# Kernel optimization log

Measured on AMD Instinct MI355X. Metric: run time of the kernel, lower is better.

The kernel has to match this reference:

```python
import jax, jax.numpy as jnp
import numpy as np

B, T_AUDIO, D_IN = 64, 500, 768
H = 1024
NUM_CHARS = 1024  # must equal H: one-hot char embeddings feed the LSTM input
SEQ_LEN = 128


def setup_inputs() -> dict:
    key = jax.random.key(0)
    ks = jax.random.split(key, 16)
    s = 1.0 / np.sqrt(H)
    u = lambda k, shape: jax.random.uniform(k, shape, jnp.float32, -s, s)
    return {
        "audio_features": jax.random.normal(ks[0], (B, T_AUDIO, D_IN), jnp.float32),
        "text_indices": jax.random.randint(ks[1], (B, SEQ_LEN), 0, NUM_CHARS),
        "W_proj": u(ks[2], (H, D_IN)), "b_proj": u(ks[3], (H,)),
        "W_ih0": u(ks[4], (4 * H, H)), "W_hh0": u(ks[5], (4 * H, H)),
        "b_ih0": u(ks[6], (4 * H,)), "b_hh0": u(ks[7], (4 * H,)),
        "W_ih1": u(ks[8], (4 * H, H)), "W_hh1": u(ks[9], (4 * H, H)),
        "b_ih1": u(ks[10], (4 * H,)), "b_hh1": u(ks[11], (4 * H,)),
        "W_out": u(ks[12], (NUM_CHARS, H)), "b_out": u(ks[13], (NUM_CHARS,)),
    }


def _lstm_cell(x, h, c, W_ih, W_hh, b_ih, b_hh):
    # PyTorch gate order: i, f, g, o
    g = x @ W_ih.T + h @ W_hh.T + b_ih + b_hh
    i, f, gg, o = jnp.split(g, 4, axis=-1)
    c = jax.nn.sigmoid(f) * c + jax.nn.sigmoid(i) * jnp.tanh(gg)
    h = jax.nn.sigmoid(o) * jnp.tanh(c)
    return h, c


def reference(audio_features, text_indices, W_proj, b_proj,
              W_ih0, W_hh0, b_ih0, b_hh0,
              W_ih1, W_hh1, b_ih1, b_hh1,
              W_out, b_out):
    # audio encoding: project then mean-pool over time -> [B, H]
    audio_enc = jnp.mean(audio_features @ W_proj.T + b_proj, axis=1)
    seq_len = text_indices.shape[1]
    # teacher-forcing inputs: step 0 = audio encoding, steps 1..L-1 = one-hot of
    # text_indices[:, 1:seq_len-1] (NUM_CHARS == H)
    one_hots = jax.nn.one_hot(text_indices[:, 1:seq_len - 1], NUM_CHARS,
                              dtype=audio_enc.dtype)  # [B, L-1, H]
    xs = jnp.concatenate([audio_enc[:, None, :], one_hots], axis=1)  # [B, L, H]
    xs = jnp.swapaxes(xs, 0, 1)  # [L, B, H]
    z = jnp.zeros((audio_enc.shape[0], H), audio_enc.dtype)

    def step(carry, x):
        h0, c0, h1, c1 = carry
        h0, c0 = _lstm_cell(x, h0, c0, W_ih0, W_hh0, b_ih0, b_hh0)
        h1, c1 = _lstm_cell(h0, h1, c1, W_ih1, W_hh1, b_ih1, b_hh1)
        return (h0, c0, h1, c1), h1

    _, hs = jax.lax.scan(step, (z, z, z, z), xs)  # hs: [L, B, H]
    outs = jnp.swapaxes(hs, 0, 1)  # [B, L, H]
    logits = outs @ W_out.T + b_out  # [B, L, NUM_CHARS]
    return logits
```

## Files before the change

kernel.cpp:

```cpp
#include <hip/hip_runtime.h>
#include <hip/hip_bf16.h>

#define HH     1024
#define BB     64
#define DIN    768
#define TAUD   500
#define LSTEPS 127
#define G4     4096
#define NB     256
#define BHH    (BB*HH)

typedef __attribute__((ext_vector_type(8))) short bf16x8;
typedef __attribute__((ext_vector_type(4))) float f32x4;
typedef unsigned short u16;
typedef unsigned long long u64;

__device__ __forceinline__ u16 f2b(float x){
  __hip_bfloat16 h = __float2bfloat16(x);
  return __builtin_bit_cast(u16, h);
}
__device__ __forceinline__ float b2f(u16 u){
  unsigned int x = ((unsigned int)u) << 16;
  return __builtin_bit_cast(float, x);
}
__device__ __forceinline__ float sig_(float x){ return 1.0f/(1.0f+__expf(-x)); }
__device__ __forceinline__ float tanh_(float x){
  float ax = fabsf(x);
  float e  = __expf(-2.0f*ax);
  float t  = (1.0f-e)/(1.0f+e);
  return x < 0.0f ? -t : t;
}

constexpr size_t O_PACK  = 0;
constexpr size_t O_WG    = O_PACK + (size_t)NB*3*16384*2;
constexpr size_t O_WOHI  = O_WG   + (size_t)NB*16384*2;
constexpr size_t O_WOLO  = O_WOHI + (size_t)HH*HH*2;
constexpr size_t O_B0P   = O_WOLO + (size_t)HH*HH*2;
constexpr size_t O_B1P   = O_B0P  + G4*4;
constexpr size_t O_G0    = O_B1P  + G4*4;
constexpr size_t O_MEAN  = O_G0   + (size_t)BB*HH*4*4;
constexpr size_t O_X0    = O_MEAN + (size_t)BB*DIN*4;
constexpr size_t O_H0R   = O_X0   + (size_t)BHH*2;
constexpr size_t O_HS    = O_H0R  + (size_t)LSTEPS*BHH*2;
constexpr size_t O_BAR   = O_HS   + (size_t)LSTEPS*BHH*2;

__global__ void init_kernel(int* bar){
  if (threadIdx.x < 512) bar[threadIdx.x] = 0;
}

__global__ void pool_kernel(const float* __restrict__ audio, float* __restrict__ mean){
  int b = blockIdx.x/3, dc = blockIdx.x%3;
  int d = dc*256 + threadIdx.x;
  const float* p = audio + (size_t)b*TAUD*DIN + d;
  float s = 0.f;
  #pragma unroll 5
  for (int t=0;t<TAUD;++t) s += p[(size_t)t*DIN];
  mean[b*DIN + d] = s*(1.0f/TAUD);
}

__global__ void project_kernel(const float* __restrict__ mean, const float* __restrict__ Wp,
                               const float* __restrict__ bp, u16* __restrict__ x0){
  __shared__ float wrow[DIN];
  __shared__ float part[256];
  int h = blockIdx.x;
  for (int i=threadIdx.x;i<DIN;i+=256) wrow[i] = Wp[(size_t)h*DIN + i];
  __syncthreads();
  int b = threadIdx.x>>2, q = threadIdx.x&3;
  const float* mr = mean + b*DIN + q*192;
  const float* wr = wrow + q*192;
  float s = 0.f;
  #pragma unroll 8
  for (int i=0;i<192;++i) s += mr[i]*wr[i];
  part[threadIdx.x] = s;
  __syncthreads();
  if (q==0){
    float v = part[threadIdx.x]+part[threadIdx.x+1]+part[threadIdx.x+2]+part[threadIdx.x+3] + bp[h];
    x0[b*HH + h] = f2b(v);
  }
}

__global__ void g0_kernel(const float* __restrict__ Wih0, const u16* __restrict__ x0bf,
                          float* __restrict__ G0p){
  __shared__ float wr[4][HH];
  __shared__ float part[256][4];
  int u = blockIdx.x;
  for (int i=threadIdx.x; i<4*HH; i+=256){
    int g = i>>10, k = i&1023;
    wr[g][k] = b2f(f2b(Wih0[(size_t)(u + g*HH)*HH + k]));
  }
  __syncthreads();
  int b = threadIdx.x>>2, q = threadIdx.x&3;
  const u16* xr = x0bf + b*HH + q*256;
  float s0=0,s1=0,s2=0,s3=0;
  for (int k=0;k<256;++k){
    float xv = b2f(xr[k]);
    s0 += xv*wr[0][q*256+k]; s1 += xv*wr[1][q*256+k];
    s2 += xv*wr[2][q*256+k]; s3 += xv*wr[3][q*256+k];
  }
  part[threadIdx.x][0]=s0; part[threadIdx.x][1]=s1;
  part[threadIdx.x][2]=s2; part[threadIdx.x][3]=s3;
  __syncthreads();
  if (threadIdx.x < 64){
    int bb = threadIdx.x;
    #pragma unroll
    for (int g=0;g<4;++g){
      float v = part[bb*4][g]+part[bb*4+1][g]+part[bb*4+2][g]+part[bb*4+3][g];
      G0p[((size_t)bb*HH + u)*4 + g] = v;
    }
  }
}

__global__ void pack_w_kernel(const float* __restrict__ Whh0, const float* __restrict__ Wih1,
                              const float* __restrict__ Whh1, u16* __restrict__ P){
  int bid = blockIdx.x, m = blockIdx.y;
  const float* src = (m==0)? Whh0 : (m==1)? Wih1 : Whh1;
  u16* dst = P + ((size_t)bid*3 + m)*16384;
  for (int e = threadIdx.x; e < 16384; e += 256){
    int r = e&31, col = (e>>5)&15, ktg = e>>9;
    int ng = bid*4 + (col&3) + (col>>2)*HH;
    dst[e] = f2b(src[(size_t)ng*HH + ktg*32 + r]);
  }
}

__global__ void pack_wg_kernel(const float* __restrict__ Wih0, u16* __restrict__ WG){
  int bid = blockIdx.x;
  for (int i = threadIdx.x; i < 16384; i += 256){
    int ch = i>>4, u = (i>>2)&3, g = i&3;
    WG[(size_t)bid*16384 + i] = f2b(Wih0[(size_t)(bid*4 + u + g*HH)*HH + ch]);
  }
}

__global__ void pack_bias_kernel(const float* bih0, const float* bhh0,
                                 const float* bih1, const float* bhh1,
                                 float* B0p, float* B1p){
  int i = blockIdx.x*256 + threadIdx.x;
  if (i < G4){
    int n = (i>>2) + (i&3)*HH;
    B0p[i] = bih0[n]+bhh0[n];
    B1p[i] = bih1[n]+bhh1[n];
  }
}

__global__ void wout_kernel(const float* __restrict__ src, u16* __restrict__ hi,
                            u16* __restrict__ lo, int n){
  int i = blockIdx.x*256+threadIdx.x, st = gridDim.x*256;
  for (;i<n;i+=st){
    float v = src[i];
    u16 h = f2b(v);
    hi[i] = h;
    lo[i] = f2b(v - b2f(h));
  }
}

__device__ __forceinline__ void sysst32(unsigned* p, unsigned v){
  __hip_atomic_store(p, v, __ATOMIC_RELAXED, __HIP_MEMORY_SCOPE_SYSTEM);
}

__device__ __forceinline__ void gridbar(int* bar, int t){
  __syncthreads();
  if (threadIdx.x==0){
    int leaf = blockIdx.x>>4;
    int a = __hip_atomic_fetch_add(&bar[leaf*32], 1, __ATOMIC_RELAXED, __HIP_MEMORY_SCOPE_SYSTEM);
    int r = a - t*16;
    if (r == 15)
      __hip_atomic_fetch_add(&bar[511], 1, __ATOMIC_RELAXED, __HIP_MEMORY_SCOPE_SYSTEM);
    if (r == 0 || r == 15){
      while (__hip_atomic_load(&bar[511], __ATOMIC_RELAXED, __HIP_MEMORY_SCOPE_SYSTEM) < (t+1)*16)
        __builtin_amdgcn_s_sleep(4);
      if (r == 0)
        __hip_atomic_store(&bar[leaf*32+16], t+1, __ATOMIC_RELAXED, __HIP_MEMORY_SCOPE_SYSTEM);
    } else {
      while (__hip_atomic_load(&bar[leaf*32+16], __ATOMIC_RELAXED, __HIP_MEMORY_SCOPE_SYSTEM) < t+1)
        __builtin_amdgcn_s_sleep(4);
    }
    asm volatile("" ::: "memory");
  }
  __syncthreads();
}

__device__ __forceinline__ f32x4 gemmK(const u16* __restrict__ A, const u16* B, f32x4 acc){
  #pragma unroll
  for (int h=0; h<2; ++h){
    bf16x8 af[16];
    #pragma unroll
    for (int i=0;i<16;++i) af[i] = *(const bf16x8*)(A + (h*16+i)*32);
    #pragma unroll
    for (int i=0;i<16;++i)
      acc = __builtin_amdgcn_mfma_f32_16x16x32_bf16(af[i], *(const bf16x8*)(B + (h*16+i)*512), acc, 0,0,0);
  }
  return acc;
}
__device__ __forceinline__ f32x4 gemm2K(const u16* __restrict__ A1, const u16* __restrict__ A2,
                                        const u16* B1, const u16* B2){
  f32x4 a1 = {0,0,0,0}, a2 = {0,0,0,0};
  #pragma unroll
  for (int h=0; h<2; ++h){
    bf16x8 af[16], ag[16];
    #pragma unroll
    for (int i=0;i<16;++i) af[i] = *(const bf16x8*)(A1 + (h*16+i)*32);
    #pragma unroll
    for (int i=0;i<16;++i) ag[i] = *(const bf16x8*)(A2 + (h*16+i)*32);
    #pragma unroll
    for (int i=0;i<16;++i){
      a1 = __builtin_amdgcn_mfma_f32_16x16x32_bf16(af[i], *(const bf16x8*)(B1 + (h*16+i)*512), a1, 0,0,0);
      a2 = __builtin_amdgcn_mfma_f32_16x16x32_bf16(ag[i], *(const bf16x8*)(B2 + (h*16+i)*512), a2, 0,0,0);
    }
  }
  return a1 + a2;
}

__device__ __forceinline__ void xpose(const f32x4 acc, float* gv, int lane){
  const int base = lane & 48, up = (lane>>2)&3, r = lane&3;
  #pragma unroll
  for (int g=0; g<4; ++g){
    int src = base | (g*4 + up);
    float v0 = __shfl(acc[0], src);
    float v1 = __shfl(acc[1], src);
    float v2 = __shfl(acc[2], src);
    float v3 = __shfl(acc[3], src);
    gv[g] = (r==0)? v0 : (r==1)? v1 : (r==2)? v2 : v3;
  }
}

__global__ void __launch_bounds__(256, 1) lstm_kernel(
    const u16* __restrict__ P, const u16* __restrict__ WG,
    const float* __restrict__ B0p, const float* __restrict__ B1p,
    const float* __restrict__ G0p, const int* __restrict__ tix,
    u16* __restrict__ h0r, u16* __restrict__ hs, int* __restrict__ bar)
{
  extern __shared__ char smem[];
  u16* Plds = (u16*)smem;
  u16* WGl  = (u16*)(smem + 98304);
  u16* tixl = (u16*)(smem + 98304 + 32768);

  const int tid  = threadIdx.x;
  const int lane = tid&63, mg = tid>>6, quad = lane>>4, colc = lane&15;
  const int bid  = blockIdx.x;

  {
    const bf16x8* gs = (const bf16x8*)(P + (size_t)bid*49152);
    bf16x8* gd = (bf16x8*)Plds;
    #pragma unroll
    for (int i=0;i<24;++i) gd[tid + i*256] = gs[tid + i*256];
    const bf16x8* ws = (const bf16x8*)(WG + (size_t)bid*16384);
    bf16x8* wd = (bf16x8*)WGl;
    #pragma unroll
    for (int i=0;i<8;++i) wd[tid + i*256] = ws[tid + i*256];
    for (int i=tid; i<BB*128; i+=256) tixl[i] = (u16)tix[(i&63)*128 + (i>>6)];
  }

  const int aoff = (mg*16 + colc)*HH + quad*8;
  const int boff = colc*32 + quad*8;
  const u16* B_hh0 = Plds + boff;
  const u16* B_ih1 = Plds + 16384 + boff;
  const u16* B_hh1 = Plds + 2*16384 + boff;

  const int bT = mg*16 + quad*4 + (lane&3);
  const int up = (lane>>2)&3;
  const int ug = bid*4 + up;
  const float4 vb0 = *(const float4*)(B0p + ug*4);
  const float4 vb1 = *(const float4*)(B1p + ug*4);
  float cc0 = 0.f, cc1 = 0.f;
  __syncthreads();

  {
    float4 g0 = *(const float4*)(G0p + ((size_t)bT*HH + ug)*4);
    float gi = g0.x+vb0.x, gg = g0.z+vb0.z, go = g0.w+vb0.w;
    cc0 = sig_(gi)*tanh_(gg);
    unsigned hv = f2b(sig_(go)*tanh_(cc0));
    unsigned ov = __shfl_xor(hv, 4);
    if ((lane&4)==0)
      sysst32((unsigned*)h0r + (bT*HH + ug)/2, hv | (ov<<16));
  }

  #pragma unroll 1
  for (int t=0;t<LSTEPS;++t){
    gridbar(bar, t);
    const u16* A1 = h0r + (size_t)t*BHH + aoff;
    {
      f32x4 acc;
      if (t==0){
        f32x4 z = {0,0,0,0};
        acc = gemmK(A1, B_ih1, z);
      } else {
        acc = gemm2K(A1, hs + (size_t)(t-1)*BHH + aoff, B_ih1, B_hh1);
      }
      float gv[4];
      xpose(acc, gv, lane);
      gv[0]+=vb1.x; gv[1]+=vb1.y; gv[2]+=vb1.z; gv[3]+=vb1.w;
      cc1 = sig_(gv[1])*cc1 + sig_(gv[0])*tanh_(gv[2]);
      unsigned hv = f2b(sig_(gv[3])*tanh_(cc1));
      unsigned ov = __shfl_xor(hv, 4);
      if ((lane&4)==0)
        sysst32((unsigned*)hs + (((size_t)t*BB + bT)*HH + ug)/2, hv | (ov<<16));
    }
    if (t < LSTEPS-1){
      f32x4 z = {0,0,0,0};
      f32x4 acc = gemmK(A1, B_hh0, z);
      float gv[4];
      xpose(acc, gv, lane);
      int ch = tixl[(t+1)*64 + bT];
      ushort4 wv = *(const ushort4*)(WGl + ch*16 + up*4);
      gv[0]+=vb0.x+b2f(wv.x); gv[1]+=vb0.y+b2f(wv.y);
      gv[2]+=vb0.z+b2f(wv.z); gv[3]+=vb0.w+b2f(wv.w);
      cc0 = sig_(gv[1])*cc0 + sig_(gv[0])*tanh_(gv[2]);
      unsigned hv = f2b(sig_(gv[3])*tanh_(cc0));
      unsigned ov = __shfl_xor(hv, 4);
      if ((lane&4)==0)
        sysst32((unsigned*)(h0r + (size_t)(t+1)*BHH) + (bT*HH + ug)/2, hv | (ov<<16));
    }
  }
}

__global__ void __launch_bounds__(512) logits_kernel(
    const u16* __restrict__ hs, const u16* __restrict__ Whi, const u16* __restrict__ Wlo,
    const float* __restrict__ bout, float* __restrict__ out)
{
  extern __shared__ u16 bsh[];
  const int tid = threadIdx.x;
  const int w = tid>>6, lane = tid&63, quad = lane>>4, col = lane&15;
  const int mt = blockIdx.x*8 + w;
  const bool active = (mt < (LSTEPS*BB)/16);
  bf16x8 afr[32];
  if (active){
    const u16* ap = hs + (size_t)(mt*16+col)*HH + quad*8;
    #pragma unroll
    for (int kt=0;kt<32;++kt) afr[kt] = *(const bf16x8*)(ap + kt*32);
  }
  const int nt0 = blockIdx.y*16;
  for (int nt=nt0; nt<nt0+16; ++nt){
    __syncthreads();
    #pragma unroll
    for (int i=0;i<8;++i){
      int cid = i*512 + tid;
      int mat = cid>>11;
      int r = (cid>>7)&15, ck = cid&127;
      const u16* src = (mat? Wlo : Whi) + (size_t)(nt*16+r)*HH + ck*8;
      *(bf16x8*)(bsh + mat*16512 + r*1032 + ck*8) = *(const bf16x8*)src;
    }
    __syncthreads();
    if (active){
      f32x4 acc = {0.f,0.f,0.f,0.f};
      const u16* bh = bsh + col*1032 + quad*8;
      const u16* bl = bsh + 16512 + col*1032 + quad*8;
      #pragma unroll 8
      for (int kt=0;kt<32;++kt){
        bf16x8 b1 = *(const bf16x8*)(bh + kt*32);
        acc = __builtin_amdgcn_mfma_f32_16x16x32_bf16(afr[kt], b1, acc, 0,0,0);
        bf16x8 b2 = *(const bf16x8*)(bl + kt*32);
        acc = __builtin_amdgcn_mfma_f32_16x16x32_bf16(afr[kt], b2, acc, 0,0,0);
      }
      float bb = bout[nt*16 + col];
      #pragma unroll
      for (int r=0;r<4;++r){
        int m = mt*16 + quad*4 + r;
        int tt = m>>6, b_ = m&63;
        out[((size_t)b_*LSTEPS + tt)*HH + nt*16 + col] = acc[r] + bb;
      }
    }
  }
}

extern "C" void kernel_launch(void* const* d_in, const int* in_sizes, int n_in,
                              void* d_out, int out_size, void* d_ws, size_t ws_size,
                              hipStream_t stream) {
  const float* audio = (const float*)d_in[0];
  const int*   tix   = (const int*)  d_in[1];
  const float* Wproj = (const float*)d_in[2];
  const float* bproj = (const float*)d_in[3];
  const float* Wih0  = (const float*)d_in[4];
  const float* Whh0  = (const float*)d_in[5];
  const float* bih0  = (const float*)d_in[6];
  const float* bhh0  = (const float*)d_in[7];
  const float* Wih1  = (const float*)d_in[8];
  const float* Whh1  = (const float*)d_in[9];
  const float* bih1  = (const float*)d_in[10];
  const float* bhh1  = (const float*)d_in[11];
  const float* Wout  = (const float*)d_in[12];
  const float* bout  = (const float*)d_in[13];
  float* out = (float*)d_out;

  char* ws = (char*)d_ws;
  u16*   wP    = (u16*)  (ws + O_PACK);
  u16*   wWG   = (u16*)  (ws + O_WG);
  u16*   wWoHi = (u16*)  (ws + O_WOHI);
  u16*   wWoLo = (u16*)  (ws + O_WOLO);
  float* wB0p  = (float*)(ws + O_B0P);
  float* wB1p  = (float*)(ws + O_B1P);
  float* wG0   = (float*)(ws + O_G0);
  float* wMean = (float*)(ws + O_MEAN);
  u16*   wX0   = (u16*)  (ws + O_X0);
  u16*   wH0R  = (u16*)  (ws + O_H0R);
  u16*   wHS   = (u16*)  (ws + O_HS);
  int*   wBar  = (int*)  (ws + O_BAR);

  init_kernel<<<1, 512, 0, stream>>>(wBar);
  pool_kernel<<<BB*3, 256, 0, stream>>>(audio, wMean);
  project_kernel<<<HH, 256, 0, stream>>>(wMean, Wproj, bproj, wX0);
  g0_kernel<<<HH, 256, 0, stream>>>(Wih0, wX0, wG0);
  pack_w_kernel<<<dim3(NB,3), 256, 0, stream>>>(Whh0, Wih1, Whh1, wP);
  pack_wg_kernel<<<NB, 256, 0, stream>>>(Wih0, wWG);
  pack_bias_kernel<<<16, 256, 0, stream>>>(bih0, bhh0, bih1, bhh1, wB0p, wB1p);
  wout_kernel<<<512, 256, 0, stream>>>(Wout, wWoHi, wWoLo, HH*HH);
  lstm_kernel<<<NB, 256, 98304 + 32768 + 16384, stream>>>(
      wP, wWG, wB0p, wB1p, wG0, tix, wH0R, wHS, wBar);
  logits_kernel<<<dim3(64,4), 512, 66048, stream>>>(wHS, wWoHi, wWoLo, bout, out);
}
```

Before: 2.438 ms.

## Replace hierarchical grid barrier with per-step flag arrays and split-layer waits

Replaces the atomic-counter tree barrier in the persistent LSTM kernel with per-block, per-step u16 ready flags for each layer. A wavefront polls all 256 flags at once with 64-bit loads. The step is reordered so layer 0's next hidden state is computed and published first. Layer 1 then waits only on the previous step's layer-1 flags, so the two layers can overlap instead of sharing one full barrier per step. This removes serialized atomic contention but adds more flag memory and two poll points per step.

```diff
diff --git a/kernel.cpp b/kernel.cpp
--- a/kernel.cpp
+++ b/kernel.cpp
@@ -42,10 +42,13 @@
 constexpr size_t O_X0    = O_MEAN + (size_t)BB*DIN*4;
 constexpr size_t O_H0R   = O_X0   + (size_t)BHH*2;
 constexpr size_t O_HS    = O_H0R  + (size_t)LSTEPS*BHH*2;
-constexpr size_t O_BAR   = O_HS   + (size_t)LSTEPS*BHH*2;
-
-__global__ void init_kernel(int* bar){
-  if (threadIdx.x < 512) bar[threadIdx.x] = 0;
+constexpr size_t O_FLA   = O_HS   + (size_t)LSTEPS*BHH*2;
+constexpr size_t O_FLB   = O_FLA  + 65536;
+
+__global__ void init_kernel(int* fl){
+  int i = blockIdx.x*256 + threadIdx.x;
+  int st = gridDim.x*256;
+  for (int k=i; k<32768; k+=st) fl[k] = 0;
 }
 
 __global__ void pool_kernel(const float* __restrict__ audio, float* __restrict__ mean){
@@ -155,27 +158,17 @@
 __device__ __forceinline__ void sysst32(unsigned* p, unsigned v){
   __hip_atomic_store(p, v, __ATOMIC_RELAXED, __HIP_MEMORY_SCOPE_SYSTEM);
 }
-
-__device__ __forceinline__ void gridbar(int* bar, int t){
-  __syncthreads();
-  if (threadIdx.x==0){
-    int leaf = blockIdx.x>>4;
-    int a = __hip_atomic_fetch_add(&bar[leaf*32], 1, __ATOMIC_RELAXED, __HIP_MEMORY_SCOPE_SYSTEM);
-    int r = a - t*16;
-    if (r == 15)
-      __hip_atomic_fetch_add(&bar[511], 1, __ATOMIC_RELAXED, __HIP_MEMORY_SCOPE_SYSTEM);
-    if (r == 0 || r == 15){
-      while (__hip_atomic_load(&bar[511], __ATOMIC_RELAXED, __HIP_MEMORY_SCOPE_SYSTEM) < (t+1)*16)
-        __builtin_amdgcn_s_sleep(4);
-      if (r == 0)
-        __hip_atomic_store(&bar[leaf*32+16], t+1, __ATOMIC_RELAXED, __HIP_MEMORY_SCOPE_SYSTEM);
-    } else {
-      while (__hip_atomic_load(&bar[leaf*32+16], __ATOMIC_RELAXED, __HIP_MEMORY_SCOPE_SYSTEM) < t+1)
-        __builtin_amdgcn_s_sleep(4);
-    }
-    asm volatile("" ::: "memory");
-  }
-  __syncthreads();
+__device__ __forceinline__ void setflag(u16* f){
+  __hip_atomic_store(f, (u16)1, __ATOMIC_RELAXED, __HIP_MEMORY_SCOPE_SYSTEM);
+}
+__device__ __forceinline__ void pollwait(const u16* f){
+  const u64* p = (const u64*)f;
+  int L = threadIdx.x & 63;
+  for (;;){
+    u64 v = __hip_atomic_load((u64*)(p + L), __ATOMIC_RELAXED, __HIP_MEMORY_SCOPE_SYSTEM);
+    if (__all(v == 0x0001000100010001ULL)) break;
+    __builtin_amdgcn_s_sleep(1);
+  }
 }
 
 __device__ __forceinline__ f32x4 gemmK(const u16* __restrict__ A, const u16* B, f32x4 acc){
@@ -226,7 +219,8 @@
     const u16* __restrict__ P, const u16* __restrict__ WG,
     const float* __restrict__ B0p, const float* __restrict__ B1p,
     const float* __restrict__ G0p, const int* __restrict__ tix,
-    u16* __restrict__ h0r, u16* __restrict__ hs, int* __restrict__ bar)
+    u16* __restrict__ h0r, u16* __restrict__ hs,
+    u16* __restrict__ flA, u16* __restrict__ flB)
 {
   extern __shared__ char smem[];
   u16* Plds = (u16*)smem;
@@ -272,18 +266,40 @@
     if ((lane&4)==0)
       sysst32((unsigned*)h0r + (bT*HH + ug)/2, hv | (ov<<16));
   }
+  __syncthreads();
+  if (tid==0) setflag(flA + bid);
 
   #pragma unroll 1
-  for (int t=0;t<LSTEPS;++t){
-    gridbar(bar, t);
-    const u16* A1 = h0r + (size_t)t*BHH + aoff;
+  for (int k=0;k<LSTEPS;++k){
+    if (tid < 64) pollwait(flA + k*256);
+    __syncthreads();
+    const u16* A1 = h0r + (size_t)k*BHH + aoff;
+    if (k < LSTEPS-1){
+      f32x4 z = {0,0,0,0};
+      f32x4 acc = gemmK(A1, B_hh0, z);
+      float gv[4];
+      xpose(acc, gv, lane);
+      int ch = tixl[(k+1)*64 + bT];
+      ushort4 wv = *(const ushort4*)(WGl + ch*16 + up*4);
+      gv[0]+=vb0.x+b2f(wv.x); gv[1]+=vb0.y+b2f(wv.y);
+      gv[2]+=vb0.z+b2f(wv.z); gv[3]+=vb0.w+b2f(wv.w);
+      cc0 = sig_(gv[1])*cc0 + sig_(gv[0])*tanh_(gv[2]);
+      unsigned hv = f2b(sig_(gv[3])*tanh_(cc0));
+      unsigned ov = __shfl_xor(hv, 4);
+      if ((lane&4)==0)
+        sysst32((unsigned*)(h0r + (size_t)(k+1)*BHH) + (bT*HH + ug)/2, hv | (ov<<16));
+    }
+    __syncthreads();
+    if (tid==0 && k < LSTEPS-1) setflag(flA + (k+1)*256 + bid);
+    if (k > 0 && tid < 64) pollwait(flB + (k-1)*256);
+    __syncthreads();
     {
       f32x4 acc;
-      if (t==0){
+      if (k==0){
         f32x4 z = {0,0,0,0};
         acc = gemmK(A1, B_ih1, z);
       } else {
-        acc = gemm2K(A1, hs + (size_t)(t-1)*BHH + aoff, B_ih1, B_hh1);
+        acc = gemm2K(A1, hs + (size_t)(k-1)*BHH + aoff, B_ih1, B_hh1);
       }
       float gv[4];
       xpose(acc, gv, lane);
@@ -292,23 +308,10 @@
       unsigned hv = f2b(sig_(gv[3])*tanh_(cc1));
       unsigned ov = __shfl_xor(hv, 4);
       if ((lane&4)==0)
-        sysst32((unsigned*)hs + (((size_t)t*BB + bT)*HH + ug)/2, hv | (ov<<16));
-    }
-    if (t < LSTEPS-1){
-      f32x4 z = {0,0,0,0};
-      f32x4 acc = gemmK(A1, B_hh0, z);
-      float gv[4];
-      xpose(acc, gv, lane);
-      int ch = tixl[(t+1)*64 + bT];
-      ushort4 wv = *(const ushort4*)(WGl + ch*16 + up*4);
-      gv[0]+=vb0.x+b2f(wv.x); gv[1]+=vb0.y+b2f(wv.y);
-      gv[2]+=vb0.z+b2f(wv.z); gv[3]+=vb0.w+b2f(wv.w);
-      cc0 = sig_(gv[1])*cc0 + sig_(gv[0])*tanh_(gv[2]);
-      unsigned hv = f2b(sig_(gv[3])*tanh_(cc0));
-      unsigned ov = __shfl_xor(hv, 4);
-      if ((lane&4)==0)
-        sysst32((unsigned*)(h0r + (size_t)(t+1)*BHH) + (bT*HH + ug)/2, hv | (ov<<16));
-    }
+        sysst32((unsigned*)hs + (((size_t)k*BB + bT)*HH + ug)/2, hv | (ov<<16));
+    }
+    __syncthreads();
+    if (tid==0) setflag(flB + k*256 + bid);
   }
 }
 
@@ -392,9 +395,10 @@
   u16*   wX0   = (u16*)  (ws + O_X0);
   u16*   wH0R  = (u16*)  (ws + O_H0R);
   u16*   wHS   = (u16*)  (ws + O_HS);
-  int*   wBar  = (int*)  (ws + O_BAR);
-
-  init_kernel<<<1, 512, 0, stream>>>(wBar);
+  u16*   wFlA  = (u16*)  (ws + O_FLA);
+  u16*   wFlB  = (u16*)  (ws + O_FLB);
+
+  init_kernel<<<64, 256, 0, stream>>>((int*)wFlA);
   pool_kernel<<<BB*3, 256, 0, stream>>>(audio, wMean);
   project_kernel<<<HH, 256, 0, stream>>>(wMean, Wproj, bproj, wX0);
   g0_kernel<<<HH, 256, 0, stream>>>(Wih0, wX0, wG0);
@@ -403,6 +407,6 @@
   pack_bias_kernel<<<16, 256, 0, stream>>>(bih0, bhh0, bih1, bhh1, wB0p, wB1p);
   wout_kernel<<<512, 256, 0, stream>>>(Wout, wWoHi, wWoLo, HH*HH);
   lstm_kernel<<<NB, 256, 98304 + 32768 + 16384, stream>>>(
-      wP, wWG, wB0p, wB1p, wG0, tix, wH0R, wHS, wBar);
+      wP, wWG, wB0p, wB1p, wG0, tix, wH0R, wHS, wFlA, wFlB);
   logits_kernel<<<dim3(64,4), 512, 66048, stream>>>(wHS, wWoHi, wWoLo, bout, out);
 }
```

After: 2.134 ms. 12.5% less time.
